# Kernel optimization log

Hardware: AMD Instinct MI355X
Metric: run time of the kernel (lower is better)

The kernel has to match this reference:

```python
import jax, jax.numpy as jnp
import numpy as np

N = 50000      # nodes
E = 800000     # edges (before self-loops)
F_IN = 128     # in_dim
H = 8          # heads
C = 16         # out_dim per head
NEG_SLOPE = 0.2
EPS = 1e-5


def setup_inputs() -> dict:
    key = jax.random.key(0)
    ks = jax.random.split(key, 8)
    x = jax.random.normal(ks[0], (N, F_IN), dtype=jnp.float32)
    edge_index = jax.random.randint(ks[1], (2, E), 0, N, dtype=jnp.int64)
    # GAT linear weight (xavier-ish scale), stored as [F_IN, H*C]
    W_gat = jax.random.normal(ks[2], (F_IN, H * C), dtype=jnp.float32) * 0.1
    att_src = jax.random.normal(ks[3], (H, C), dtype=jnp.float32) * 0.1
    att_dst = jax.random.normal(ks[4], (H, C), dtype=jnp.float32) * 0.1
    bias_gat = jnp.zeros((H * C,), dtype=jnp.float32)
    W_skip = jax.random.normal(ks[5], (F_IN, H * C), dtype=jnp.float32) * 0.1
    gamma = jnp.ones((H * C,), dtype=jnp.float32)
    beta = jnp.zeros((H * C,), dtype=jnp.float32)
    return {"x": x, "edge_index": edge_index, "W_gat": W_gat,
            "att_src": att_src, "att_dst": att_dst, "bias_gat": bias_gat,
            "W_skip": W_skip, "gamma": gamma, "beta": beta}


def reference(x, edge_index, W_gat, att_src, att_dst, bias_gat, W_skip, gamma, beta):
    # PyG GATConv default: add self-loops
    loop = jnp.arange(N, dtype=edge_index.dtype)
    src = jnp.concatenate([edge_index[0], loop])  # [E+N]
    dst = jnp.concatenate([edge_index[1], loop])  # [E+N]

    h = (x @ W_gat).reshape(N, H, C)              # [N,H,C]
    a_src = jnp.sum(h * att_src, axis=-1)          # [N,H]
    a_dst = jnp.sum(h * att_dst, axis=-1)          # [N,H]

    e = jax.nn.leaky_relu(a_src[src] + a_dst[dst], NEG_SLOPE)   # [E+N,H]
    # segment softmax over destination nodes
    e_max = jax.ops.segment_max(e, dst, num_segments=N)         # [N,H]
    e_exp = jnp.exp(e - e_max[dst])
    denom = jax.ops.segment_sum(e_exp, dst, num_segments=N)     # [N,H]
    alpha = e_exp / denom[dst]                                   # [E+N,H]

    msg = alpha[:, :, None] * h[src]                             # [E+N,H,C]
    gat_out = jax.ops.segment_sum(msg, dst, num_segments=N)     # [N,H,C]
    gat_out = gat_out.reshape(N, H * C) + bias_gat

    skip_out = x @ W_skip                                        # [N,H*C]
    z = gat_out + 0.1 * skip_out

    mu = jnp.mean(z, axis=-1, keepdims=True)
    var = jnp.mean((z - mu) ** 2, axis=-1, keepdims=True)
    z = (z - mu) * jax.lax.rsqrt(var + EPS) * gamma + beta
    return jax.nn.elu(z)  # dropout is identity in eval mode
```

## Files before the change

### kernel.cpp

```cpp
#include <hip/hip_runtime.h>
#include <hip/hip_bf16.h>

#define N_NODES 50000
#define N_EDGES 800000
#define F_IN    128
#define HC      128

typedef __attribute__((ext_vector_type(8))) short bf16x8;
typedef __attribute__((ext_vector_type(4))) float f32x4;

__device__ __forceinline__ float bf2f(unsigned int u16) {
    return __uint_as_float(u16 << 16);
}
__device__ __forceinline__ unsigned int f2bf(float f) {
    unsigned int u = __float_as_uint(f);
    return (u + 0x7fffu + ((u >> 16) & 1u)) >> 16;
}

__global__ __launch_bounds__(256) void k_pc(
    const int* __restrict__ dst,
    const float* __restrict__ Wg, const float* __restrict__ Ws,
    unsigned short* __restrict__ Bfrag, int* __restrict__ counts)
{
    const int bid = blockIdx.x;
    if (bid < 3125) {
        const int i = bid * 256 + threadIdx.x;
        if (i < N_EDGES) atomicAdd(&counts[dst[i]], 1);
    } else {
        const int g = (bid - 3125) * 256 + threadIdx.x;
        if (g < 4096) {
            const int lane = g & 63;
            const int kq = (g >> 6) & 3;
            const int nt = g >> 8;
            const int c = nt * 16 + (lane & 15);
            const int kbase = kq * 32 + (lane >> 4) * 8;
            const float* Wsel = (c < 128) ? (Wg + c) : (Ws + c - 128);
            unsigned int pk[4];
#pragma unroll
            for (int p = 0; p < 4; p++) {
                const float v0 = Wsel[(size_t)(kbase + 2 * p) * HC];
                const float v1 = Wsel[(size_t)(kbase + 2 * p + 1) * HC];
                pk[p] = f2bf(v0) | (f2bf(v1) << 16);
            }
            *(uint4*)(Bfrag + (size_t)g * 8) = make_uint4(pk[0], pk[1], pk[2], pk[3]);
        }
    }
}

__global__ __launch_bounds__(256) void k_scanA(const int* __restrict__ counts,
                                               int* __restrict__ row_start,
                                               int* __restrict__ bsum) {
    __shared__ int s[256];
    const int tid = threadIdx.x;
    const int base = blockIdx.x * 1024 + tid * 4;
    int v[4]; int t = 0;
#pragma unroll
    for (int j = 0; j < 4; j++) {
        int idx = base + j;
        v[j] = (idx < N_NODES) ? (counts[idx] + 1) : 0;
        t += v[j];
    }
    s[tid] = t;
    __syncthreads();
    for (int off = 1; off < 256; off <<= 1) {
        int add = (tid >= off) ? s[tid - off] : 0;
        __syncthreads();
        s[tid] += add;
        __syncthreads();
    }
    int excl = s[tid] - t;
#pragma unroll
    for (int j = 0; j < 4; j++) {
        int idx = base + j;
        if (idx < N_NODES) row_start[idx] = excl;
        excl += v[j];
    }
    if (tid == 255) bsum[blockIdx.x] = s[255];
}

__global__ void k_scanB(int* bsum, int nb) {
    int tid = threadIdx.x;
    int v = (tid < nb) ? bsum[tid] : 0;
    int orig = v;
    for (int off = 1; off < 64; off <<= 1) {
        int y = __shfl_up(v, off);
        if (tid >= off) v += y;
    }
    if (tid < nb) bsum[tid] = v - orig;
}

__global__ void k_scanC(int* __restrict__ row_start, const int* __restrict__ bsum,
                        int* __restrict__ cursor) {
    int i = blockIdx.x * 256 + threadIdx.x;
    if (i < N_NODES) {
        int rs = row_start[i] + bsum[i >> 10];
        row_start[i] = rs;
        cursor[i] = rs;
    }
}

__global__ __launch_bounds__(256) void k_lf(
    const float* __restrict__ x,
    const unsigned short* __restrict__ Bfrag,
    const float* __restrict__ att_s,
    const float* __restrict__ att_d,
    const float* __restrict__ bias,
    unsigned short* __restrict__ h_bf, unsigned int* __restrict__ z0b,
    float* __restrict__ a_src, float* __restrict__ a_dst,
    const int* __restrict__ src, const int* __restrict__ dst,
    int* cursor, int* __restrict__ csr)
{
    const int bid = blockIdx.x;
    const int tid = threadIdx.x;
    const bool is_lin = (bid % 5 == 0) && (bid < 3910);

    if (!is_lin) {
        const int fid = (bid < 3910) ? (bid - (bid + 4) / 5) : (bid - 782);
        const int i = fid * 256 + tid;
        if (i < N_EDGES + N_NODES) {
            int s, d;
            if (i < N_EDGES) { s = src[i]; d = dst[i]; }
            else             { s = d = i - N_EDGES; }
            const int slot = atomicAdd(&cursor[d], 1);
            csr[slot] = s;
        }
        return;
    }

    __shared__ unsigned short sA[16 * 64 * 8];
    const int lin = bid / 5;
    const int lane = tid & 63;
    const int w = tid >> 6;
    const int nbase = lin * 64;

#pragma unroll
    for (int it = 0; it < 4; it++) {
        const int p = it * 256 + tid;
        const int node = p >> 4;
        const int kg = p & 15;
        const int gn = nbase + node;
        float v[8];
        if (gn < N_NODES) {
            float4 u0 = *(const float4*)(x + (size_t)gn * F_IN + kg * 8);
            float4 u1 = *(const float4*)(x + (size_t)gn * F_IN + kg * 8 + 4);
            v[0] = u0.x; v[1] = u0.y; v[2] = u0.z; v[3] = u0.w;
            v[4] = u1.x; v[5] = u1.y; v[6] = u1.z; v[7] = u1.w;
        } else {
#pragma unroll
            for (int j = 0; j < 8; j++) v[j] = 0.f;
        }
        const int mt = node >> 4, lm = node & 15;
        const int kq = kg >> 2, quad = kg & 3;
        uint4 pk;
        pk.x = f2bf(v[0]) | (f2bf(v[1]) << 16);
        pk.y = f2bf(v[2]) | (f2bf(v[3]) << 16);
        pk.z = f2bf(v[4]) | (f2bf(v[5]) << 16);
        pk.w = f2bf(v[6]) | (f2bf(v[7]) << 16);
        *(uint4*)(sA + ((size_t)((mt * 4 + kq) * 64 + quad * 16 + lm)) * 8) = pk;
    }
    __syncthreads();

    const bf16x8* Bf = (const bf16x8*)Bfrag;
    f32x4 acc[4][4];
#pragma unroll
    for (int mt = 0; mt < 4; mt++)
#pragma unroll
        for (int nt = 0; nt < 4; nt++)
            acc[mt][nt] = (f32x4){0.f, 0.f, 0.f, 0.f};

#pragma unroll
    for (int kq = 0; kq < 4; kq++) {
        bf16x8 aF[4], bF[4];
#pragma unroll
        for (int nt = 0; nt < 4; nt++)
            bF[nt] = Bf[(size_t)(((w * 4 + nt) * 4 + kq) * 64 + lane)];
#pragma unroll
        for (int mt = 0; mt < 4; mt++)
            aF[mt] = *(const bf16x8*)(sA + ((size_t)((mt * 4 + kq) * 64 + lane)) * 8);
#pragma unroll
        for (int mt = 0; mt < 4; mt++)
#pragma unroll
            for (int nt = 0; nt < 4; nt++)
                acc[mt][nt] = __builtin_amdgcn_mfma_f32_16x16x32_bf16(
                    aF[mt], bF[nt], acc[mt][nt], 0, 0, 0);
    }

    const int row4 = (lane >> 4) * 4;
    const int cl = lane & 15;
#pragma unroll
    for (int mt = 0; mt < 4; mt++) {
#pragma unroll
        for (int nt = 0; nt < 4; nt++) {
            const int c = w * 64 + nt * 16 + cl;
            f32x4 d = acc[mt][nt];
            if (c < 128) {
                const float asv = att_s[c];
                const float adv = att_d[c];
                float ps[4], pd[4];
#pragma unroll
                for (int r = 0; r < 4; r++) { ps[r] = d[r] * asv; pd[r] = d[r] * adv; }
#pragma unroll
                for (int m = 1; m <= 8; m <<= 1) {
#pragma unroll
                    for (int r = 0; r < 4; r++) {
                        ps[r] += __shfl_xor(ps[r], m);
                        pd[r] += __shfl_xor(pd[r], m);
                    }
                }
                const int head = w * 4 + nt;
#pragma unroll
                for (int r = 0; r < 4; r++) {
                    const int gn = nbase + mt * 16 + row4 + r;
                    if (gn < N_NODES) {
                        h_bf[(size_t)gn * HC + c] = (unsigned short)f2bf(d[r]);
                        if (cl == 0) {
                            a_src[gn * 8 + head] = ps[r];
                            a_dst[gn * 8 + head] = pd[r];
                        }
                    }
                }
            } else {
                const int cz = c - 128;
                const float bv = bias[cz];
#pragma unroll
                for (int r = 0; r < 4; r++) {
                    const int gn = nbase + mt * 16 + row4 + r;
                    const float val = 0.1f * d[r] + bv;
                    const float oth = __shfl_xor(val, 1);
                    if ((cl & 1) == 0 && gn < N_NODES) {
                        z0b[(size_t)gn * 64 + (cz >> 1)] =
                            f2bf(val) | (f2bf(oth) << 16);
                    }
                }
            }
        }
    }
}

__global__ __launch_bounds__(256) void k_agg(
    const uint2* __restrict__ h2,
    const uint2* __restrict__ z0b,
    const float* __restrict__ a_src, const float* __restrict__ a_dst,
    const int* __restrict__ row_start, const int* __restrict__ counts,
    const int* __restrict__ csr,
    const float* __restrict__ gamma, const float* __restrict__ beta,
    float* __restrict__ out)
{
    const int tid = threadIdx.x;
    const int lane = tid & 63;
    const int l = lane & 31;
    const int n = blockIdx.x * 8 + ((tid >> 6) << 1) + (lane >> 5);
    const int head = l >> 2;

    const float adn = a_dst[n * 8 + head];
    const int rs = row_start[n];
    const int cnt = counts[n] + 1;

    float d_acc = 0.f, a0 = 0.f, a1 = 0.f, a2 = 0.f, a3 = 0.f;
    for (int i = 0; i < cnt; i += 4) {
        int s[4]; float ae[4], mk[4]; uint2 hp[4];
#pragma unroll
        for (int j = 0; j < 4; j++) {
            const int e = i + j;
            const int ec = (e < cnt) ? e : (cnt - 1);
            mk[j] = (e < cnt) ? 1.f : 0.f;
            s[j] = csr[rs + ec];
        }
#pragma unroll
        for (int j = 0; j < 4; j++) ae[j] = a_src[s[j] * 8 + head];
#pragma unroll
        for (int j = 0; j < 4; j++) hp[j] = h2[(size_t)s[j] * 32 + l];
#pragma unroll
        for (int j = 0; j < 4; j++) {
            float e = ae[j] + adn;
            e = (e > 0.f) ? e : 0.2f * e;
            const float wgt = __expf(e) * mk[j];
            d_acc += wgt;
            a0 += wgt * bf2f(hp[j].x & 0xffffu);
            a1 += wgt * bf2f(hp[j].x >> 16);
            a2 += wgt * bf2f(hp[j].y & 0xffffu);
            a3 += wgt * bf2f(hp[j].y >> 16);
        }
    }
    const float inv = 1.0f / d_acc;
    const uint2 zp = z0b[(size_t)n * 32 + l];
    float y0 = a0 * inv + bf2f(zp.x & 0xffffu);
    float y1 = a1 * inv + bf2f(zp.x >> 16);
    float y2 = a2 * inv + bf2f(zp.y & 0xffffu);
    float y3 = a3 * inv + bf2f(zp.y >> 16);

    float ss = y0 + y1 + y2 + y3;
#pragma unroll
    for (int off = 1; off < 32; off <<= 1) ss += __shfl_xor(ss, off);
    const float mu = ss * (1.0f / 128.0f);
    const float d0 = y0 - mu, d1 = y1 - mu, d2 = y2 - mu, d3 = y3 - mu;
    float vs = d0 * d0 + d1 * d1 + d2 * d2 + d3 * d3;
#pragma unroll
    for (int off = 1; off < 32; off <<= 1) vs += __shfl_xor(vs, off);
    const float rstd = rsqrtf(vs * (1.0f / 128.0f) + 1e-5f);

    const float4 gv = *(const float4*)(gamma + l * 4);
    const float4 bv = *(const float4*)(beta + l * 4);
    float o0 = d0 * rstd * gv.x + bv.x;
    float o1 = d1 * rstd * gv.y + bv.y;
    float o2 = d2 * rstd * gv.z + bv.z;
    float o3 = d3 * rstd * gv.w + bv.w;
    o0 = (o0 > 0.f) ? o0 : (__expf(o0) - 1.0f);
    o1 = (o1 > 0.f) ? o1 : (__expf(o1) - 1.0f);
    o2 = (o2 > 0.f) ? o2 : (__expf(o2) - 1.0f);
    o3 = (o3 > 0.f) ? o3 : (__expf(o3) - 1.0f);

    *(float4*)(out + (size_t)n * HC + l * 4) = make_float4(o0, o1, o2, o3);
}

extern "C" void kernel_launch(void* const* d_in, const int* in_sizes, int n_in,
                              void* d_out, int out_size, void* d_ws, size_t ws_size,
                              hipStream_t stream) {
    const float* x   = (const float*)d_in[0];
    const int*   ei  = (const int*)d_in[1];
    const float* Wg  = (const float*)d_in[2];
    const float* as_ = (const float*)d_in[3];
    const float* ad_ = (const float*)d_in[4];
    const float* bg  = (const float*)d_in[5];
    const float* Wsk = (const float*)d_in[6];
    const float* gm  = (const float*)d_in[7];
    const float* bt  = (const float*)d_in[8];
    float* out = (float*)d_out;

    char* wsb = (char*)d_ws;
    unsigned short* h_bf  = (unsigned short*)wsb;
    unsigned int*   z0b   = (unsigned int*)(wsb + 12800000);
    float*          a_src = (float*)(wsb + 25600000);
    float*          a_dst = (float*)(wsb + 27200000);
    unsigned short* Bfrag = (unsigned short*)(wsb + 28800000);
    int*   counts = (int*)(wsb + 28865536);
    int*   row_st = (int*)(wsb + 29065728);
    int*   cursor = (int*)(wsb + 29265920);
    int*   bsum   = (int*)(wsb + 29466112);
    int*   csr    = (int*)(wsb + 29467136);

    const int* src = ei;
    const int* dst = ei + N_EDGES;

    hipMemsetAsync(counts, 0, 50048 * sizeof(int), stream);
    k_pc   <<<3141, 256, 0, stream>>>(dst, Wg, Wsk, Bfrag, counts);
    k_scanA<<<49, 256, 0, stream>>>(counts, row_st, bsum);
    k_scanB<<<1, 64, 0, stream>>>(bsum, 49);
    k_scanC<<<(N_NODES + 255) / 256, 256, 0, stream>>>(row_st, bsum, cursor);
    k_lf   <<<4103, 256, 0, stream>>>(x, Bfrag, as_, ad_, bg, h_bf, z0b,
                                      a_src, a_dst, src, dst, cursor, csr);
    k_agg  <<<N_NODES / 8, 256, 0, stream>>>((const uint2*)h_bf, (const uint2*)z0b,
                                             a_src, a_dst, row_st, counts, csr,
                                             gm, bt, out);
}
```

Before: 226.6 us.

## Build CSR with shared-memory partitioned histograms instead of global atomics

```diff
diff --git a/kernel.cpp b/kernel.cpp
--- a/kernel.cpp
+++ b/kernel.cpp
@@ -5,6 +5,10 @@
 #define N_EDGES 800000
 #define F_IN    128
 #define HC      128
+#define NR      8
+#define RSZ     6250
+#define NCH     16
+#define CHSZ    50000
 
 typedef __attribute__((ext_vector_type(8))) short bf16x8;
 typedef __attribute__((ext_vector_type(4))) float f32x4;
@@ -17,24 +21,40 @@
     return (u + 0x7fffu + ((u >> 16) & 1u)) >> 16;
 }
 
-__global__ __launch_bounds__(256) void k_pc(
+__global__ __launch_bounds__(256) void k_hist(
     const int* __restrict__ dst,
     const float* __restrict__ Wg, const float* __restrict__ Ws,
-    unsigned short* __restrict__ Bfrag, int* __restrict__ counts)
+    unsigned short* __restrict__ Bfrag, int* __restrict__ part)
 {
     const int bid = blockIdx.x;
-    if (bid < 3125) {
-        const int i = bid * 256 + threadIdx.x;
-        if (i < N_EDGES) atomicAdd(&counts[dst[i]], 1);
+    const int tid = threadIdx.x;
+    if (bid < 128) {
+        __shared__ int hist[RSZ];
+        const int r = bid & 7, c = bid >> 3;
+        const int nb = r * RSZ;
+        for (int i = tid; i < RSZ; i += 256) hist[i] = 0;
+        __syncthreads();
+        const int4* d4 = (const int4*)(dst + c * CHSZ);
+        for (int i = tid; i < CHSZ / 4; i += 256) {
+            const int4 v = d4[i];
+            int b;
+            b = v.x - nb; if ((unsigned)b < (unsigned)RSZ) atomicAdd(&hist[b], 1);
+            b = v.y - nb; if ((unsigned)b < (unsigned)RSZ) atomicAdd(&hist[b], 1);
+            b = v.z - nb; if ((unsigned)b < (unsigned)RSZ) atomicAdd(&hist[b], 1);
+            b = v.w - nb; if ((unsigned)b < (unsigned)RSZ) atomicAdd(&hist[b], 1);
+        }
+        __syncthreads();
+        for (int i = tid; i < RSZ; i += 256)
+            part[(size_t)(nb + i) * NCH + c] = hist[i];
     } else {
-        const int g = (bid - 3125) * 256 + threadIdx.x;
+        const int g = (bid - 128) * 256 + tid;
         if (g < 4096) {
             const int lane = g & 63;
             const int kq = (g >> 6) & 3;
             const int nt = g >> 8;
-            const int c = nt * 16 + (lane & 15);
+            const int cc = nt * 16 + (lane & 15);
             const int kbase = kq * 32 + (lane >> 4) * 8;
-            const float* Wsel = (c < 128) ? (Wg + c) : (Ws + c - 128);
+            const float* Wsel = (cc < 128) ? (Wg + cc) : (Ws + cc - 128);
             unsigned int pk[4];
 #pragma unroll
             for (int p = 0; p < 4; p++) {
@@ -45,6 +65,25 @@
             *(uint4*)(Bfrag + (size_t)g * 8) = make_uint4(pk[0], pk[1], pk[2], pk[3]);
         }
     }
+}
+
+__global__ __launch_bounds__(256) void k_merge(int* __restrict__ part,
+                                               int* __restrict__ counts)
+{
+    const int n = blockIdx.x * 256 + threadIdx.x;
+    if (n >= N_NODES) return;
+    int4* p = (int4*)(part + (size_t)n * NCH);
+    int4 v0 = p[0], v1 = p[1], v2 = p[2], v3 = p[3];
+    int vv[16] = {v0.x, v0.y, v0.z, v0.w, v1.x, v1.y, v1.z, v1.w,
+                  v2.x, v2.y, v2.z, v2.w, v3.x, v3.y, v3.z, v3.w};
+    int run = 0;
+#pragma unroll
+    for (int c = 0; c < 16; c++) { const int t = vv[c]; vv[c] = run; run += t; }
+    counts[n] = run;
+    p[0] = make_int4(vv[0], vv[1], vv[2], vv[3]);
+    p[1] = make_int4(vv[4], vv[5], vv[6], vv[7]);
+    p[2] = make_int4(vv[8], vv[9], vv[10], vv[11]);
+    p[3] = make_int4(vv[12], vv[13], vv[14], vv[15]);
 }
 
 __global__ __launch_bounds__(256) void k_scanA(const int* __restrict__ counts,
@@ -90,12 +129,12 @@
 }
 
 __global__ void k_scanC(int* __restrict__ row_start, const int* __restrict__ bsum,
-                        int* __restrict__ cursor) {
+                        const int* __restrict__ counts, int* __restrict__ csr) {
     int i = blockIdx.x * 256 + threadIdx.x;
     if (i < N_NODES) {
         int rs = row_start[i] + bsum[i >> 10];
         row_start[i] = rs;
-        cursor[i] = rs;
+        csr[rs + counts[i]] = i;
     }
 }
 
@@ -108,27 +147,41 @@
     unsigned short* __restrict__ h_bf, unsigned int* __restrict__ z0b,
     float* __restrict__ a_src, float* __restrict__ a_dst,
     const int* __restrict__ src, const int* __restrict__ dst,
-    int* cursor, int* __restrict__ csr)
+    const int* __restrict__ row_start, const int* __restrict__ part,
+    int* __restrict__ csr)
 {
+    __shared__ __align__(16) int smem[RSZ];
     const int bid = blockIdx.x;
     const int tid = threadIdx.x;
-    const bool is_lin = (bid % 5 == 0) && (bid < 3910);
-
-    if (!is_lin) {
-        const int fid = (bid < 3910) ? (bid - (bid + 4) / 5) : (bid - 782);
-        const int i = fid * 256 + tid;
-        if (i < N_EDGES + N_NODES) {
-            int s, d;
-            if (i < N_EDGES) { s = src[i]; d = dst[i]; }
-            else             { s = d = i - N_EDGES; }
-            const int slot = atomicAdd(&cursor[d], 1);
-            csr[slot] = s;
+    int lin = -1, r = 0, c = 0;
+    if (bid < 256) {
+        const int g = bid >> 4, pos = bid & 15;
+        if (pos < 8) { r = pos; c = g; }
+        else lin = g * 8 + (pos - 8);
+    } else {
+        lin = 128 + (bid - 256);
+    }
+
+    if (lin < 0) {
+        const int nb = r * RSZ;
+        for (int b = tid; b < RSZ; b += 256)
+            smem[b] = row_start[nb + b] + part[(size_t)(nb + b) * NCH + c];
+        __syncthreads();
+        const int4* d4 = (const int4*)(dst + c * CHSZ);
+        const int4* s4 = (const int4*)(src + c * CHSZ);
+        for (int i = tid; i < CHSZ / 4; i += 256) {
+            const int4 dv = d4[i];
+            const int4 sv = s4[i];
+            int b;
+            b = dv.x - nb; if ((unsigned)b < (unsigned)RSZ) csr[atomicAdd(&smem[b], 1)] = sv.x;
+            b = dv.y - nb; if ((unsigned)b < (unsigned)RSZ) csr[atomicAdd(&smem[b], 1)] = sv.y;
+            b = dv.z - nb; if ((unsigned)b < (unsigned)RSZ) csr[atomicAdd(&smem[b], 1)] = sv.z;
+            b = dv.w - nb; if ((unsigned)b < (unsigned)RSZ) csr[atomicAdd(&smem[b], 1)] = sv.w;
         }
         return;
     }
 
-    __shared__ unsigned short sA[16 * 64 * 8];
-    const int lin = bid / 5;
+    unsigned short* sA = (unsigned short*)smem;
     const int lane = tid & 63;
     const int w = tid >> 6;
     const int nbase = lin * 64;
@@ -191,41 +244,41 @@
     for (int mt = 0; mt < 4; mt++) {
 #pragma unroll
         for (int nt = 0; nt < 4; nt++) {
-            const int c = w * 64 + nt * 16 + cl;
+            const int cc = w * 64 + nt * 16 + cl;
             f32x4 d = acc[mt][nt];
-            if (c < 128) {
-                const float asv = att_s[c];
-                const float adv = att_d[c];
+            if (cc < 128) {
+                const float asv = att_s[cc];
+                const float adv = att_d[cc];
                 float ps[4], pd[4];
 #pragma unroll
-                for (int r = 0; r < 4; r++) { ps[r] = d[r] * asv; pd[r] = d[r] * adv; }
+                for (int rr = 0; rr < 4; rr++) { ps[rr] = d[rr] * asv; pd[rr] = d[rr] * adv; }
 #pragma unroll
                 for (int m = 1; m <= 8; m <<= 1) {
 #pragma unroll
-                    for (int r = 0; r < 4; r++) {
-                        ps[r] += __shfl_xor(ps[r], m);
-                        pd[r] += __shfl_xor(pd[r], m);
+                    for (int rr = 0; rr < 4; rr++) {
+                        ps[rr] += __shfl_xor(ps[rr], m);
+                        pd[rr] += __shfl_xor(pd[rr], m);
                     }
                 }
                 const int head = w * 4 + nt;
 #pragma unroll
-                for (int r = 0; r < 4; r++) {
-                    const int gn = nbase + mt * 16 + row4 + r;
+                for (int rr = 0; rr < 4; rr++) {
+                    const int gn = nbase + mt * 16 + row4 + rr;
                     if (gn < N_NODES) {
-                        h_bf[(size_t)gn * HC + c] = (unsigned short)f2bf(d[r]);
+                        h_bf[(size_t)gn * HC + cc] = (unsigned short)f2bf(d[rr]);
                         if (cl == 0) {
-                            a_src[gn * 8 + head] = ps[r];
-                            a_dst[gn * 8 + head] = pd[r];
+                            a_src[gn * 8 + head] = ps[rr];
+                            a_dst[gn * 8 + head] = pd[rr];
                         }
                     }
                 }
             } else {
-                const int cz = c - 128;
+                const int cz = cc - 128;
                 const float bv = bias[cz];
 #pragma unroll
-                for (int r = 0; r < 4; r++) {
-                    const int gn = nbase + mt * 16 + row4 + r;
-                    const float val = 0.1f * d[r] + bv;
+                for (int rr = 0; rr < 4; rr++) {
+                    const int gn = nbase + mt * 16 + row4 + rr;
+                    const float val = 0.1f * d[rr] + bv;
                     const float oth = __shfl_xor(val, 1);
                     if ((cl & 1) == 0 && gn < N_NODES) {
                         z0b[(size_t)gn * 64 + (cz >> 1)] =
@@ -335,20 +388,20 @@
     unsigned short* Bfrag = (unsigned short*)(wsb + 28800000);
     int*   counts = (int*)(wsb + 28865536);
     int*   row_st = (int*)(wsb + 29065728);
-    int*   cursor = (int*)(wsb + 29265920);
-    int*   bsum   = (int*)(wsb + 29466112);
-    int*   csr    = (int*)(wsb + 29467136);
+    int*   bsum   = (int*)(wsb + 29265920);
+    int*   csr    = (int*)(wsb + 29266944);
+    int*   part   = (int*)(wsb + 32666944);
 
     const int* src = ei;
     const int* dst = ei + N_EDGES;
 
-    hipMemsetAsync(counts, 0, 50048 * sizeof(int), stream);
-    k_pc   <<<3141, 256, 0, stream>>>(dst, Wg, Wsk, Bfrag, counts);
+    k_hist <<<144, 256, 0, stream>>>(dst, Wg, Wsk, Bfrag, part);
+    k_merge<<<196, 256, 0, stream>>>(part, counts);
     k_scanA<<<49, 256, 0, stream>>>(counts, row_st, bsum);
     k_scanB<<<1, 64, 0, stream>>>(bsum, 49);
-    k_scanC<<<(N_NODES + 255) / 256, 256, 0, stream>>>(row_st, bsum, cursor);
-    k_lf   <<<4103, 256, 0, stream>>>(x, Bfrag, as_, ad_, bg, h_bf, z0b,
-                                      a_src, a_dst, src, dst, cursor, csr);
+    k_scanC<<<196, 256, 0, stream>>>(row_st, bsum, counts, csr);
+    k_lf   <<<910, 256, 0, stream>>>(x, Bfrag, as_, ad_, bg, h_bf, z0b,
+                                     a_src, a_dst, src, dst, row_st, part, csr);
     k_agg  <<<N_NODES / 8, 256, 0, stream>>>((const uint2*)h_bf, (const uint2*)z0b,
                                              a_src, a_dst, row_st, counts, csr,
                                              gm, bt, out);
```

Result: faster. 213.2 us (-5.9%).
